# Performance work log

Hardware: AMD Instinct MI355X
Metric: run time of the kernel (lower is better)

## Reference

```python
import jax, jax.numpy as jnp
import numpy as np

B, T, P, C, H = 2, 2048, 2048, 1024, 16  # batch, new tokens, cached tokens, n_embd, n_head
HD = C // H  # head_dim = 64


def setup_inputs() -> dict:
    key = jax.random.key(0)
    ks = jax.random.split(key, 5)
    return {
        "x": jax.random.normal(ks[0], (B, T, C), dtype=jnp.float32),
        "k_cache": jax.random.normal(ks[1], (B, P, C), dtype=jnp.float32),
        "v_cache": jax.random.normal(ks[2], (B, P, C), dtype=jnp.float32),
        "W_attn": jax.random.normal(ks[3], (C, 3 * C), dtype=jnp.float32) * 0.02,
        "W_proj": jax.random.normal(ks[4], (C, C), dtype=jnp.float32) * 0.02,
    }


def reference(x, k_cache, v_cache, W_attn, W_proj):
    # c_attn (no bias): qkv projection, then split into q, k_rem, v_rem
    qkv = x @ W_attn                      # [B, T, 3C]
    q, k_rem, v_rem = jnp.split(qkv, 3, axis=2)
    # KV-cache concat along time
    k_full = jnp.concatenate([k_cache, k_rem], axis=1)  # [B, S, C], S = P + T
    v_full = jnp.concatenate([v_cache, v_rem], axis=1)
    S = P + T
    # reshape to heads
    qh = q.reshape(B, T, H, HD).transpose(0, 2, 1, 3)       # [B, H, T, HD]
    kh = k_full.reshape(B, S, H, HD).transpose(0, 2, 1, 3)  # [B, H, S, HD]
    vh = v_full.reshape(B, S, H, HD).transpose(0, 2, 1, 3)  # [B, H, S, HD]
    # full attention matrix (module explicitly disables flash)
    att = jnp.einsum("bhqd,bhkd->bhqk", qh, kh) * (1.0 / np.sqrt(HD))  # [B,H,T,S]
    # cache-offset causal mask: query global position = P + i attends to key j <= P + i
    mask = jnp.arange(S)[None, :] <= (P + jnp.arange(T))[:, None]  # [T, S]
    att = jnp.where(mask[None, None], att, -jnp.inf)
    att = jax.nn.softmax(att, axis=-1)
    # dropout p=0.0 (inference) -> no-op
    y = jnp.einsum("bhqk,bhkd->bhqd", att, vh)  # [B, H, T, HD]
    y = y.transpose(0, 2, 1, 3).reshape(B, T, C)
    y = y @ W_proj  # c_proj, no bias; resid dropout p=0 -> no-op
    return (y, k_full, v_full)
```

## Files before the change

### kernel.cpp

```cpp
#include <hip/hip_runtime.h>

#define BB 2
#define TT 2048
#define PP 2048
#define CC 1024
#define HH 16
#define SS 4096

typedef unsigned short u16;
typedef __attribute__((ext_vector_type(8))) short s16x8;
typedef __attribute__((ext_vector_type(4))) float f32x4;
typedef __attribute__((ext_vector_type(4))) unsigned short u16x4;

#define QSCALE 0.18033688011112042f

__device__ __forceinline__ u16 f2bf(float f) {
  unsigned u = __float_as_uint(f);
  u += 0x7fff + ((u >> 16) & 1);
  return (u16)(u >> 16);
}

__device__ __forceinline__ u16 p2bf(float f) {
  return (u16)((__float_as_uint(f) + 0x8000u) >> 16);
}

__global__ __launch_bounds__(256) void cvt_f32_bf16(const float* __restrict__ src,
                                                    u16* __restrict__ dst) {
  size_t i = ((size_t)blockIdx.x * 256 + threadIdx.x) * 4;
  f32x4 v = *(const f32x4*)(src + i);
  u16x4 o = { f2bf(v[0]), f2bf(v[1]), f2bf(v[2]), f2bf(v[3]) };
  *(u16x4*)(dst + i) = o;
}

__global__ __launch_bounds__(256) void transpose_w_bf16(const float* __restrict__ src,
                                                        u16* __restrict__ dst,
                                                        int rows, int cols) {
  __shared__ float tile[64][65];
  int r0 = blockIdx.y * 64, c0 = blockIdx.x * 64;
  int tx = threadIdx.x & 63, ty = threadIdx.x >> 6;
#pragma unroll
  for (int i = 0; i < 16; i++) {
    int r = ty + i * 4;
    tile[r][tx] = src[(size_t)(r0 + r) * cols + c0 + tx];
  }
  __syncthreads();
#pragma unroll
  for (int i = 0; i < 16; i++) {
    int cc = ty + i * 4;
    dst[(size_t)(c0 + cc) * rows + r0 + tx] = f2bf(tile[tx][cc]);
  }
}

__global__ __launch_bounds__(256) void cache_copy(const float* __restrict__ kc,
                                                  const float* __restrict__ vc,
                                                  float* __restrict__ kf,
                                                  float* __restrict__ vf,
                                                  u16* __restrict__ kb) {
  size_t flat = ((size_t)blockIdx.x * 256 + threadIdx.x) * 4;
  int b = (int)(flat >> 21);
  size_t dsto = flat + (size_t)b * (TT * CC);
  f32x4 kv = *(const f32x4*)(kc + flat);
  f32x4 vv = *(const f32x4*)(vc + flat);
  *(f32x4*)(kf + dsto) = kv;
  *(f32x4*)(vf + dsto) = vv;
  u16x4 k4 = { f2bf(kv[0]), f2bf(kv[1]), f2bf(kv[2]), f2bf(kv[3]) };
  *(u16x4*)(kb + dsto) = k4;
}

__global__ __launch_bounds__(256) void vT_cache_kernel(const float* __restrict__ vc,
                                                       u16* __restrict__ vTb) {
  __shared__ float tile[64][65];
  int bh = blockIdx.y, b = bh >> 4, h = bh & 15;
  int p0 = blockIdx.x * 64;
  int tx = threadIdx.x & 63, ty = threadIdx.x >> 6;
#pragma unroll
  for (int i = 0; i < 16; i++) {
    int p = ty + i * 4;
    tile[p][tx] = vc[(size_t)(b * PP + p0 + p) * CC + h * 64 + tx];
  }
  __syncthreads();
#pragma unroll
  for (int i = 0; i < 16; i++) {
    int d = ty + i * 4;
    vTb[(size_t)((b * HH + h) * 64 + d) * SS + p0 + tx] = f2bf(tile[tx][d]);
  }
}

__global__ __launch_bounds__(256) void vT_rem_kernel(const float* __restrict__ vf,
                                                     u16* __restrict__ vTb) {
  __shared__ float tile[64][65];
  int bh = blockIdx.y, b = bh >> 4, h = bh & 15;
  int p0 = blockIdx.x * 64;
  int tx = threadIdx.x & 63, ty = threadIdx.x >> 6;
#pragma unroll
  for (int i = 0; i < 16; i++) {
    int p = ty + i * 4;
    tile[p][tx] = vf[(size_t)(b * SS + PP + p0 + p) * CC + h * 64 + tx];
  }
  __syncthreads();
#pragma unroll
  for (int i = 0; i < 16; i++) {
    int d = ty + i * 4;
    vTb[(size_t)((b * HH + h) * 64 + d) * SS + PP + p0 + tx] = f2bf(tile[tx][d]);
  }
}

__global__ __launch_bounds__(256) void gemm_bt(const u16* __restrict__ A,
                                               const u16* __restrict__ BT,
                                               int N, int mode,
                                               float* __restrict__ out0,
                                               u16* __restrict__ qb,
                                               float* __restrict__ kf,
                                               u16* __restrict__ kb,
                                               float* __restrict__ vf) {
  __shared__ u16 As[128 * 72];
  __shared__ u16 Bs[128 * 72];
  const int m0 = blockIdx.y * 128, n0 = blockIdx.x * 128;
  const int tid = threadIdx.x, lane = tid & 63, wave = tid >> 6;
  const int wm = wave & 1, wn = wave >> 1;
  const int c = lane & 15, quad = lane >> 4;
  const int chunk = tid & 7, rp = tid >> 3;

  f32x4 acc[4][4] = {};

  for (int k0 = 0; k0 < 1024; k0 += 64) {
#pragma unroll
    for (int it = 0; it < 4; it++) {
      int r = it * 32 + rp;
      *(s16x8*)&As[r * 72 + chunk * 8] =
          *(const s16x8*)(A + (size_t)(m0 + r) * 1024 + k0 + chunk * 8);
      *(s16x8*)&Bs[r * 72 + chunk * 8] =
          *(const s16x8*)(BT + (size_t)(n0 + r) * 1024 + k0 + chunk * 8);
    }
    __syncthreads();
#pragma unroll
    for (int kc = 0; kc < 64; kc += 32) {
      s16x8 af[4], bf[4];
#pragma unroll
      for (int i = 0; i < 4; i++) {
        af[i] = *(const s16x8*)&As[(wm * 64 + i * 16 + c) * 72 + kc + quad * 8];
        bf[i] = *(const s16x8*)&Bs[(wn * 64 + i * 16 + c) * 72 + kc + quad * 8];
      }
#pragma unroll
      for (int mi = 0; mi < 4; mi++)
#pragma unroll
        for (int ni = 0; ni < 4; ni++)
          acc[mi][ni] = __builtin_amdgcn_mfma_f32_16x16x32_bf16(af[mi], bf[ni], acc[mi][ni], 0, 0, 0);
    }
    __syncthreads();
  }

#pragma unroll
  for (int mi = 0; mi < 4; mi++) {
#pragma unroll
    for (int ni = 0; ni < 4; ni++) {
      f32x4 v = acc[mi][ni];
      int gmb = m0 + wm * 64 + mi * 16 + quad * 4;
      int gn = n0 + wn * 64 + ni * 16 + c;
      if (mode == 0) {
#pragma unroll
        for (int r = 0; r < 4; r++)
          out0[(size_t)(gmb + r) * N + gn] = v[r];
      } else {
        int region = n0 >> 10;
        if (region == 0) {
#pragma unroll
          for (int r = 0; r < 4; r++)
            qb[(size_t)(gmb + r) * 1024 + gn] = f2bf(v[r] * QSCALE);
        } else if (region == 1) {
          int ccol = gn - 1024;
#pragma unroll
          for (int r = 0; r < 4; r++) {
            int gm = gmb + r, b = gm >> 11, t = gm & 2047;
            size_t off = (size_t)b * (SS * CC) + (size_t)(PP + t) * CC + ccol;
            kf[off] = v[r];
            kb[off] = f2bf(v[r]);
          }
        } else {
          int ccol = gn - 2048;
#pragma unroll
          for (int r = 0; r < 4; r++) {
            int gm = gmb + r, b = gm >> 11, t = gm & 2047;
            vf[(size_t)b * (SS * CC) + (size_t)(PP + t) * CC + ccol] = v[r];
          }
        }
      }
    }
  }
}

__global__ __launch_bounds__(512, 4) void attn_kernel(const u16* __restrict__ qb,
                                                      const u16* __restrict__ kb,
                                                      const u16* __restrict__ vT,
                                                      u16* __restrict__ yb) {
  __shared__ u16 Ks[2][64 * 72];
  __shared__ u16 Vs[2][64 * 72];
  __shared__ u16 Ps[8][16 * 72];
  const int L = blockIdx.x;
  const int xcd = L & 7, rest = L >> 3;
  const int qt = 15 - (rest >> 2);
  const int bh = (xcd << 2) | (rest & 3);
  const int b = bh >> 4, h = bh & 15;
  const int q0 = qt * 128;
  const int tid = threadIdx.x, lane = tid & 63, wave = tid >> 6;
  const int c = lane & 15, quad = lane >> 4;
  const int chunk = tid & 7, rp = tid >> 3;

  const int s_end = PP + q0 + 128;

  const u16* kptr = kb + (size_t)(b * SS + rp) * 1024 + h * 64 + chunk * 8;
  const u16* vptr = vT + (size_t)((b * HH + h) * 64 + rp) * SS + chunk * 8;

  {
    s16x8 k0 = *(const s16x8*)kptr;
    s16x8 v0 = *(const s16x8*)vptr;
    *(s16x8*)&Ks[0][rp * 72 + chunk * 8] = k0;
    *(s16x8*)&Vs[0][rp * 72 + chunk * 8] = v0;
  }

  const short ov = (c == 0) ? (short)0x3F80 : (short)0;
  const s16x8 ones = { ov, ov, ov, ov, ov, ov, ov, ov };

  s16x8 qf[2];
  {
    int qr = q0 + wave * 16 + c;
    qf[0] = *(const s16x8*)(qb + (size_t)(b * TT + qr) * 1024 + h * 64 + quad * 8);
    qf[1] = *(const s16x8*)(qb + (size_t)(b * TT + qr) * 1024 + h * 64 + 32 + quad * 8);
  }

  f32x4 o[5] = {};
  float m = -1e30f;
  u16* Pw = Ps[wave];
  s16x8 kreg, vreg;

  int cur = 0;
  for (int s0 = 0; s0 < s_end; s0 += 64, cur ^= 1) {
    __syncthreads();

    const bool more = (s0 + 64 < s_end);
    if (more) {
      kptr += 64 * 1024;
      vptr += 64;
      kreg = *(const s16x8*)kptr;
      vreg = *(const s16x8*)vptr;
    }

    const u16* Kc = Ks[cur];
    const u16* Vc = Vs[cur];

    f32x4 sc[4];
    __builtin_amdgcn_s_setprio(1);
#pragma unroll
    for (int nt = 0; nt < 4; nt++) {
      s16x8 kf0 = *(const s16x8*)&Kc[(nt * 16 + c) * 72 + quad * 8];
      s16x8 kf1 = *(const s16x8*)&Kc[(nt * 16 + c) * 72 + 32 + quad * 8];
      f32x4 z = { 0.f, 0.f, 0.f, 0.f };
      z = __builtin_amdgcn_mfma_f32_16x16x32_bf16(qf[0], kf0, z, 0, 0, 0);
      z = __builtin_amdgcn_mfma_f32_16x16x32_bf16(qf[1], kf1, z, 0, 0, 0);
      sc[nt] = z;
    }
    __builtin_amdgcn_s_setprio(0);

    s16x8 vf0[4], vf1[4];
#pragma unroll
    for (int dt = 0; dt < 4; dt++) {
      vf0[dt] = *(const s16x8*)&Vc[(dt * 16 + c) * 72 + quad * 8];
      vf1[dt] = *(const s16x8*)&Vc[(dt * 16 + c) * 72 + 32 + quad * 8];
    }

    const int diag = s0 - (PP + q0);
    if (diag >= 0) {
#pragma unroll
      for (int nt = 0; nt < 4; nt++) {
        int col = nt * 16 + c + diag;
#pragma unroll
        for (int r = 0; r < 4; r++) {
          int rq = wave * 16 + quad * 4 + r;
          if (col > rq) sc[nt][r] = -1e30f;
        }
      }
    }

    float lm = -1e30f;
#pragma unroll
    for (int nt = 0; nt < 4; nt++)
      lm = fmaxf(lm, fmaxf(fmaxf(sc[nt][0], sc[nt][1]),
                           fmaxf(sc[nt][2], sc[nt][3])));
    if (__any(lm > m + 8.0f)) {
#pragma unroll
      for (int off = 1; off < 64; off <<= 1)
        lm = fmaxf(lm, __shfl_xor(lm, off, 64));
      float alpha = __builtin_amdgcn_exp2f(m - lm);
      m = lm;
#pragma unroll
      for (int dt = 0; dt < 5; dt++)
#pragma unroll
        for (int r = 0; r < 4; r++) o[dt][r] *= alpha;
    }

#pragma unroll
    for (int nt = 0; nt < 4; nt++)
#pragma unroll
      for (int r = 0; r < 4; r++)
        Pw[(quad * 4 + r) * 72 + nt * 16 + c] =
            p2bf(__builtin_amdgcn_exp2f(sc[nt][r] - m));
    s16x8 pa0 = *(const s16x8*)&Pw[c * 72 + quad * 8];
    s16x8 pa1 = *(const s16x8*)&Pw[c * 72 + 32 + quad * 8];

    if (more) {
      *(s16x8*)&Ks[cur ^ 1][rp * 72 + chunk * 8] = kreg;
      *(s16x8*)&Vs[cur ^ 1][rp * 72 + chunk * 8] = vreg;
    }

    __builtin_amdgcn_s_setprio(1);
#pragma unroll
    for (int dt = 0; dt < 4; dt++) {
      o[dt] = __builtin_amdgcn_mfma_f32_16x16x32_bf16(pa0, vf0[dt], o[dt], 0, 0, 0);
      o[dt] = __builtin_amdgcn_mfma_f32_16x16x32_bf16(pa1, vf1[dt], o[dt], 0, 0, 0);
    }
    o[4] = __builtin_amdgcn_mfma_f32_16x16x32_bf16(pa0, ones, o[4], 0, 0, 0);
    o[4] = __builtin_amdgcn_mfma_f32_16x16x32_bf16(pa1, ones, o[4], 0, 0, 0);
    __builtin_amdgcn_s_setprio(0);
  }

#pragma unroll
  for (int r = 0; r < 4; r++) {
    float l = __shfl(o[4][r], (lane & 48), 64);
    float inv = 1.0f / l;
    int qr = q0 + wave * 16 + quad * 4 + r;
#pragma unroll
    for (int dt = 0; dt < 4; dt++)
      yb[(size_t)(b * TT + qr) * 1024 + h * 64 + dt * 16 + c] = f2bf(o[dt][r] * inv);
  }
}

extern "C" void kernel_launch(void* const* d_in, const int* in_sizes, int n_in,
                              void* d_out, int out_size, void* d_ws, size_t ws_size,
                              hipStream_t stream) {
  const float* x       = (const float*)d_in[0];
  const float* k_cache = (const float*)d_in[1];
  const float* v_cache = (const float*)d_in[2];
  const float* W_attn  = (const float*)d_in[3];
  const float* W_proj  = (const float*)d_in[4];

  float* out_y = (float*)d_out;
  float* out_k = out_y + (size_t)BB * TT * CC;
  float* out_v = out_k + (size_t)BB * SS * CC;

  u16* xb  = (u16*)d_ws;
  u16* WaT = xb  + 4194304;
  u16* WpT = WaT + 3145728;
  u16* qb  = WpT + 1048576;
  u16* kb  = qb  + 4194304;
  u16* vT  = kb  + 8388608;
  u16* yb  = vT  + 8388608;

  cvt_f32_bf16<<<dim3(4096), dim3(256), 0, stream>>>(x, xb);
  transpose_w_bf16<<<dim3(48, 16), dim3(256), 0, stream>>>(W_attn, WaT, 1024, 3072);
  transpose_w_bf16<<<dim3(16, 16), dim3(256), 0, stream>>>(W_proj, WpT, 1024, 1024);
  cache_copy<<<dim3(4096), dim3(256), 0, stream>>>(k_cache, v_cache, out_k, out_v, kb);
  vT_cache_kernel<<<dim3(32, 32), dim3(256), 0, stream>>>(v_cache, vT);
  gemm_bt<<<dim3(24, 32), dim3(256), 0, stream>>>(xb, WaT, 3072, 1, nullptr, qb, out_k, kb, out_v);
  vT_rem_kernel<<<dim3(32, 32), dim3(256), 0, stream>>>(out_v, vT);
  attn_kernel<<<dim3(512), dim3(512), 0, stream>>>(qb, kb, vT, yb);
  gemm_bt<<<dim3(8, 32), dim3(256), 0, stream>>>(yb, WpT, 1024, 0, out_y, nullptr, nullptr, nullptr, nullptr);
}
```

Measured before the change: 324.6 us.

## Use direct global-to-LDS loads with XOR-swizzled shared layouts in GEMM and attention

Replaces register-staged global loads followed by LDS stores with global_load_lds direct transfers in both the projection GEMM and the attention kernel. Drops the padded 72-stride LDS rows in favour of 64-stride rows with an XOR swizzle, so fragment reads stay bank-conflict free without padding, and swizzles the per-wave P buffer too. This removes VGPR staging and the extra LDS write instructions and shrinks LDS use. The GEMM still has no double buffering, so load latency is exposed behind the barrier, and correctness depends on the swizzle matching the direct-load lane mapping.

```diff
diff --git a/kernel.cpp b/kernel.cpp
--- a/kernel.cpp
+++ b/kernel.cpp
@@ -8,9 +8,14 @@
 #define SS 4096
 
 typedef unsigned short u16;
+typedef unsigned int u32;
 typedef __attribute__((ext_vector_type(8))) short s16x8;
 typedef __attribute__((ext_vector_type(4))) float f32x4;
 typedef __attribute__((ext_vector_type(4))) unsigned short u16x4;
+
+#define GLOAD16(g, l)                                                                   \
+  __builtin_amdgcn_global_load_lds((const __attribute__((address_space(1))) u32*)(g),   \
+                                   (__attribute__((address_space(3))) u32*)(l), 16, 0, 0)
 
 #define QSCALE 0.18033688011112042f
 
@@ -113,24 +118,26 @@
                                                float* __restrict__ kf,
                                                u16* __restrict__ kb,
                                                float* __restrict__ vf) {
-  __shared__ u16 As[128 * 72];
-  __shared__ u16 Bs[128 * 72];
+  __shared__ u16 As[128 * 64];
+  __shared__ u16 Bs[128 * 64];
   const int m0 = blockIdx.y * 128, n0 = blockIdx.x * 128;
   const int tid = threadIdx.x, lane = tid & 63, wave = tid >> 6;
   const int wm = wave & 1, wn = wave >> 1;
   const int c = lane & 15, quad = lane >> 4;
-  const int chunk = tid & 7, rp = tid >> 3;
+  const int srow = lane >> 3;
+  const int scol = (lane & 7) ^ (srow & 7);
+  const int rkey = (c & 7) << 3;
 
   f32x4 acc[4][4] = {};
 
   for (int k0 = 0; k0 < 1024; k0 += 64) {
+    __syncthreads();
 #pragma unroll
     for (int it = 0; it < 4; it++) {
-      int r = it * 32 + rp;
-      *(s16x8*)&As[r * 72 + chunk * 8] =
-          *(const s16x8*)(A + (size_t)(m0 + r) * 1024 + k0 + chunk * 8);
-      *(s16x8*)&Bs[r * 72 + chunk * 8] =
-          *(const s16x8*)(BT + (size_t)(n0 + r) * 1024 + k0 + chunk * 8);
+      int chunk = it * 4 + wave;
+      int row = chunk * 8 + srow;
+      GLOAD16(A + (size_t)(m0 + row) * 1024 + k0 + scol * 8, &As[chunk * 512]);
+      GLOAD16(BT + (size_t)(n0 + row) * 1024 + k0 + scol * 8, &Bs[chunk * 512]);
     }
     __syncthreads();
 #pragma unroll
@@ -138,8 +145,8 @@
       s16x8 af[4], bf[4];
 #pragma unroll
       for (int i = 0; i < 4; i++) {
-        af[i] = *(const s16x8*)&As[(wm * 64 + i * 16 + c) * 72 + kc + quad * 8];
-        bf[i] = *(const s16x8*)&Bs[(wn * 64 + i * 16 + c) * 72 + kc + quad * 8];
+        af[i] = *(const s16x8*)&As[(((wm * 64 + i * 16 + c) << 6) + kc + quad * 8) ^ rkey];
+        bf[i] = *(const s16x8*)&Bs[(((wn * 64 + i * 16 + c) << 6) + kc + quad * 8) ^ rkey];
       }
 #pragma unroll
       for (int mi = 0; mi < 4; mi++)
@@ -147,7 +154,6 @@
         for (int ni = 0; ni < 4; ni++)
           acc[mi][ni] = __builtin_amdgcn_mfma_f32_16x16x32_bf16(af[mi], bf[ni], acc[mi][ni], 0, 0, 0);
     }
-    __syncthreads();
   }
 
 #pragma unroll
@@ -193,9 +199,9 @@
                                                       const u16* __restrict__ kb,
                                                       const u16* __restrict__ vT,
                                                       u16* __restrict__ yb) {
-  __shared__ u16 Ks[2][64 * 72];
-  __shared__ u16 Vs[2][64 * 72];
-  __shared__ u16 Ps[8][16 * 72];
+  __shared__ u16 Ks[2][64 * 64];
+  __shared__ u16 Vs[2][64 * 64];
+  __shared__ u16 Ps[8][16 * 64];
   const int L = blockIdx.x;
   const int xcd = L & 7, rest = L >> 3;
   const int qt = 15 - (rest >> 2);
@@ -204,19 +210,17 @@
   const int q0 = qt * 128;
   const int tid = threadIdx.x, lane = tid & 63, wave = tid >> 6;
   const int c = lane & 15, quad = lane >> 4;
-  const int chunk = tid & 7, rp = tid >> 3;
+  const int srow = lane >> 3;
+  const int scol = (lane & 7) ^ (srow & 7);
+  const int rkey = (c & 7) << 3;
 
   const int s_end = PP + q0 + 128;
 
-  const u16* kptr = kb + (size_t)(b * SS + rp) * 1024 + h * 64 + chunk * 8;
-  const u16* vptr = vT + (size_t)((b * HH + h) * 64 + rp) * SS + chunk * 8;
-
-  {
-    s16x8 k0 = *(const s16x8*)kptr;
-    s16x8 v0 = *(const s16x8*)vptr;
-    *(s16x8*)&Ks[0][rp * 72 + chunk * 8] = k0;
-    *(s16x8*)&Vs[0][rp * 72 + chunk * 8] = v0;
-  }
+  const u16* kg = kb + (size_t)(b * SS + wave * 8 + srow) * 1024 + h * 64 + scol * 8;
+  const u16* vg = vT + ((size_t)bh * 64 + wave * 8 + srow) * SS + scol * 8;
+
+  GLOAD16(kg, &Ks[0][wave * 512]);
+  GLOAD16(vg, &Vs[0][wave * 512]);
 
   const short ov = (c == 0) ? (short)0x3F80 : (short)0;
   const s16x8 ones = { ov, ov, ov, ov, ov, ov, ov, ov };
@@ -231,18 +235,14 @@
   f32x4 o[5] = {};
   float m = -1e30f;
   u16* Pw = Ps[wave];
-  s16x8 kreg, vreg;
 
   int cur = 0;
   for (int s0 = 0; s0 < s_end; s0 += 64, cur ^= 1) {
     __syncthreads();
 
-    const bool more = (s0 + 64 < s_end);
-    if (more) {
-      kptr += 64 * 1024;
-      vptr += 64;
-      kreg = *(const s16x8*)kptr;
-      vreg = *(const s16x8*)vptr;
+    if (s0 + 64 < s_end) {
+      GLOAD16(kg + (size_t)(s0 + 64) * 1024, &Ks[cur ^ 1][wave * 512]);
+      GLOAD16(vg + (s0 + 64), &Vs[cur ^ 1][wave * 512]);
     }
 
     const u16* Kc = Ks[cur];
@@ -252,8 +252,8 @@
     __builtin_amdgcn_s_setprio(1);
 #pragma unroll
     for (int nt = 0; nt < 4; nt++) {
-      s16x8 kf0 = *(const s16x8*)&Kc[(nt * 16 + c) * 72 + quad * 8];
-      s16x8 kf1 = *(const s16x8*)&Kc[(nt * 16 + c) * 72 + 32 + quad * 8];
+      s16x8 kf0 = *(const s16x8*)&Kc[(((nt * 16 + c) << 6) + quad * 8) ^ rkey];
+      s16x8 kf1 = *(const s16x8*)&Kc[(((nt * 16 + c) << 6) + 32 + quad * 8) ^ rkey];
       f32x4 z = { 0.f, 0.f, 0.f, 0.f };
       z = __builtin_amdgcn_mfma_f32_16x16x32_bf16(qf[0], kf0, z, 0, 0, 0);
       z = __builtin_amdgcn_mfma_f32_16x16x32_bf16(qf[1], kf1, z, 0, 0, 0);
@@ -264,8 +264,8 @@
     s16x8 vf0[4], vf1[4];
 #pragma unroll
     for (int dt = 0; dt < 4; dt++) {
-      vf0[dt] = *(const s16x8*)&Vc[(dt * 16 + c) * 72 + quad * 8];
-      vf1[dt] = *(const s16x8*)&Vc[(dt * 16 + c) * 72 + 32 + quad * 8];
+      vf0[dt] = *(const s16x8*)&Vc[(((dt * 16 + c) << 6) + quad * 8) ^ rkey];
+      vf1[dt] = *(const s16x8*)&Vc[(((dt * 16 + c) << 6) + 32 + quad * 8) ^ rkey];
     }
 
     const int diag = s0 - (PP + q0);
@@ -302,15 +302,11 @@
     for (int nt = 0; nt < 4; nt++)
 #pragma unroll
       for (int r = 0; r < 4; r++)
-        Pw[(quad * 4 + r) * 72 + nt * 16 + c] =
+        Pw[(((quad * 4 + r) << 6) + nt * 16 + c) ^ (quad << 4)] =
             p2bf(__builtin_amdgcn_exp2f(sc[nt][r] - m));
-    s16x8 pa0 = *(const s16x8*)&Pw[c * 72 + quad * 8];
-    s16x8 pa1 = *(const s16x8*)&Pw[c * 72 + 32 + quad * 8];
-
-    if (more) {
-      *(s16x8*)&Ks[cur ^ 1][rp * 72 + chunk * 8] = kreg;
-      *(s16x8*)&Vs[cur ^ 1][rp * 72 + chunk * 8] = vreg;
-    }
+    const int pkey = (c >> 2) << 4;
+    s16x8 pa0 = *(const s16x8*)&Pw[((c << 6) + quad * 8) ^ pkey];
+    s16x8 pa1 = *(const s16x8*)&Pw[((c << 6) + 32 + quad * 8) ^ pkey];
 
     __builtin_amdgcn_s_setprio(1);
 #pragma unroll
```

New measurement: 316.7 us. 1.02x faster.
